# Performance work log

Measured on AMD Instinct MI355X. Metric: run time of the kernel, lower is better.

## Reference

```python
import jax, jax.numpy as jnp
import numpy as np

H_RATIO = 0.33  # matches init_kwargs h_ratio
EPS = 1e-12     # F.normalize default eps


def setup_inputs() -> dict:
    key = jax.random.key(0)
    x = jax.random.normal(key, (64, 2048, 24, 12), dtype=jnp.float32)
    return {"x": x}


def reference(x):
    b, c, h, w = x.shape
    rh = round(H_RATIO * h)  # number of top-energy rows to drop (static)
    # per-sample spatial activation energy, summed over channels: (b, h*w)
    act = jnp.sum(x * x, axis=1).reshape(b, h * w)
    # L2 normalize per sample (faithful to F.normalize; order-preserving anyway)
    norm = jnp.sqrt(jnp.sum(act * act, axis=1, keepdims=True))
    act = act / jnp.maximum(norm, EPS)
    act = act.reshape(b, h, w)
    # per-row max over width -> (b, h); take indices of the rh largest rows
    max_act = jnp.max(act, axis=2)
    ind = jnp.argsort(max_act, axis=1)[:, -rh:]  # (b, rh)
    # row mask: ones everywhere, zero at the top-rh rows per sample
    mask = jnp.ones((b, h), dtype=x.dtype)
    mask = mask.at[jnp.arange(b)[:, None], ind].set(0.0)  # (b, h)
    # broadcast over channels and width (equiv. to the repeat_interleave chain)
    return x * mask[:, None, :, None]
```

## Files before the change

kernel.cpp:

```cpp
#include <hip/hip_runtime.h>

#define B   64
#define C   2048
#define H   24
#define W   12
#define S   (H * W)
#define S4  (S / 4)
#define NCH 32
#define CCH (C / NCH)
#define RH  8

__global__ __launch_bounds__(288) void k_energy_copy(const float* __restrict__ x,
                                                     float* __restrict__ out,
                                                     float* __restrict__ part) {
    const int chunk = blockIdx.x;
    const int b     = blockIdx.y;
    const int t     = threadIdx.x;
    const int f     = t % S4;
    const int g     = t / S4;

    const size_t base4 = (size_t)b * C * S4 + (size_t)chunk * CCH * S4;
    const float4* __restrict__ x4 = (const float4*)x + base4;
    float4* __restrict__       o4 = (float4*)out + base4;

    float4 acc = {0.f, 0.f, 0.f, 0.f};
    #pragma unroll 4
    for (int c = g; c < CCH; c += 4) {
        float4 v = x4[c * S4 + f];
        o4[c * S4 + f] = v;
        acc.x += v.x * v.x;
        acc.y += v.y * v.y;
        acc.z += v.z * v.z;
        acc.w += v.w * v.w;
    }

    __shared__ float4 sm4[4][S4];
    sm4[g][f] = acc;
    __syncthreads();

    const float* sm = (const float*)sm4;
    float sum = sm[0 * S + t] + sm[1 * S + t] + sm[2 * S + t] + sm[3 * S + t];
    part[((size_t)b * NCH + chunk) * S + t] = sum;
}

__global__ __launch_bounds__(288) void k_select(const float* __restrict__ part,
                                                int* __restrict__ drop) {
    const int b = blockIdx.x;
    const int t = threadIdx.x;

    __shared__ float act[S];
    __shared__ float rm[H];

    const float* p = part + (size_t)b * NCH * S + t;
    float sum = 0.f;
    #pragma unroll
    for (int ch = 0; ch < NCH; ch++) sum += p[(size_t)ch * S];
    act[t] = sum;
    __syncthreads();

    if (t < H) {
        float m = act[t * W];
        #pragma unroll
        for (int w = 1; w < W; w++) m = fmaxf(m, act[t * W + w]);
        rm[t] = m;
    }
    __syncthreads();

    if (t < H) {
        const float mt = rm[t];
        int cnt = 0;
        #pragma unroll
        for (int j = 0; j < H; j++) {
            float mj = rm[j];
            if (mj > mt || (mj == mt && j > t)) cnt++;
        }
        drop[b * H + t] = (cnt < RH) ? 1 : 0;
    }
}

__global__ __launch_bounds__(256) void k_zero(float* __restrict__ out,
                                              const int* __restrict__ drop) {
    const int h = blockIdx.x;
    const int b = blockIdx.y;
    if (!drop[b * H + h]) return;

    float4* __restrict__ o4 = (float4*)out + (size_t)b * C * S4 + h * (W / 4);
    const float4 z = {0.f, 0.f, 0.f, 0.f};
    for (int i = threadIdx.x; i < C * (W / 4); i += 256) {
        int c = i / 3;
        int q = i - c * 3;
        o4[(size_t)c * S4 + q] = z;
    }
}

extern "C" void kernel_launch(void* const* d_in, const int* in_sizes, int n_in,
                              void* d_out, int out_size, void* d_ws, size_t ws_size,
                              hipStream_t stream) {
    const float* x   = (const float*)d_in[0];
    float*       out = (float*)d_out;

    float* part = (float*)d_ws;
    int*   drop = (int*)((char*)d_ws + (size_t)B * NCH * S * sizeof(float));

    k_energy_copy<<<dim3(NCH, B), 288, 0, stream>>>(x, out, part);
    k_select<<<B, 288, 0, stream>>>(part, drop);
    k_zero<<<dim3(H, B), 256, 0, stream>>>(out, drop);
}
```

Baseline: 309.1 us.

## Split energy pass from copy and fuse row masking into a second streaming copy

Result: faster. 278.3 us (-10.0%).

```diff
diff --git a/kernel.cpp b/kernel.cpp
--- a/kernel.cpp
+++ b/kernel.cpp
@@ -6,41 +6,38 @@
 #define W   12
 #define S   (H * W)
 #define S4  (S / 4)
+#define W4  (W / 4)
 #define NCH 32
 #define CCH (C / NCH)
 #define RH  8
 
-__global__ __launch_bounds__(288) void k_energy_copy(const float* __restrict__ x,
-                                                     float* __restrict__ out,
-                                                     float* __restrict__ part) {
+typedef float f4 __attribute__((ext_vector_type(4)));
+
+__global__ __launch_bounds__(288) void k_energy(const float* __restrict__ x,
+                                                float* __restrict__ part) {
     const int chunk = blockIdx.x;
     const int b     = blockIdx.y;
     const int t     = threadIdx.x;
     const int f     = t % S4;
     const int g     = t / S4;
 
-    const size_t base4 = (size_t)b * C * S4 + (size_t)chunk * CCH * S4;
-    const float4* __restrict__ x4 = (const float4*)x + base4;
-    float4* __restrict__       o4 = (float4*)out + base4;
+    const f4* __restrict__ x4 =
+        (const f4*)x + (size_t)(b * C + chunk * CCH) * S4;
 
-    float4 acc = {0.f, 0.f, 0.f, 0.f};
-    #pragma unroll 4
-    for (int c = g; c < CCH; c += 4) {
-        float4 v = x4[c * S4 + f];
-        o4[c * S4 + f] = v;
-        acc.x += v.x * v.x;
-        acc.y += v.y * v.y;
-        acc.z += v.z * v.z;
-        acc.w += v.w * v.w;
+    f4 acc = {0.f, 0.f, 0.f, 0.f};
+    #pragma unroll
+    for (int k = 0; k < CCH / 4; ++k) {
+        f4 v = x4[t + S * k];
+        acc += v * v;
     }
 
-    __shared__ float4 sm4[4][S4];
+    __shared__ f4 sm4[4][S4];
     sm4[g][f] = acc;
     __syncthreads();
 
     const float* sm = (const float*)sm4;
-    float sum = sm[0 * S + t] + sm[1 * S + t] + sm[2 * S + t] + sm[3 * S + t];
-    part[((size_t)b * NCH + chunk) * S + t] = sum;
+    part[((size_t)b * NCH + chunk) * S + t] =
+        sm[0 * S + t] + sm[1 * S + t] + sm[2 * S + t] + sm[3 * S + t];
 }
 
 __global__ __launch_bounds__(288) void k_select(const float* __restrict__ part,
@@ -78,18 +75,24 @@
     }
 }
 
-__global__ __launch_bounds__(256) void k_zero(float* __restrict__ out,
-                                              const int* __restrict__ drop) {
-    const int h = blockIdx.x;
-    const int b = blockIdx.y;
-    if (!drop[b * H + h]) return;
+__global__ __launch_bounds__(288) void k_mask_copy(const float* __restrict__ x,
+                                                   float* __restrict__ out,
+                                                   const int* __restrict__ drop) {
+    const int chunk = blockIdx.x;
+    const int b     = blockIdx.y;
+    const int t     = threadIdx.x;
+    const int h     = (t % S4) / W4;
+    const float keep = (drop[b * H + h] == 0) ? 1.0f : 0.0f;
 
-    float4* __restrict__ o4 = (float4*)out + (size_t)b * C * S4 + h * (W / 4);
-    const float4 z = {0.f, 0.f, 0.f, 0.f};
-    for (int i = threadIdx.x; i < C * (W / 4); i += 256) {
-        int c = i / 3;
-        int q = i - c * 3;
-        o4[(size_t)c * S4 + q] = z;
+    const size_t base4 = (size_t)(b * C + chunk * CCH) * S4;
+    const f4* __restrict__ x4 = (const f4*)x + base4;
+    f4* __restrict__       o4 = (f4*)out + base4;
+
+    #pragma unroll
+    for (int k = 0; k < CCH / 4; ++k) {
+        f4 v = x4[t + S * k];
+        f4 r = v * keep;
+        __builtin_nontemporal_store(r, &o4[t + S * k]);
     }
 }
 
@@ -102,7 +105,7 @@
     float* part = (float*)d_ws;
     int*   drop = (int*)((char*)d_ws + (size_t)B * NCH * S * sizeof(float));
 
-    k_energy_copy<<<dim3(NCH, B), 288, 0, stream>>>(x, out, part);
+    k_energy<<<dim3(NCH, B), 288, 0, stream>>>(x, part);
     k_select<<<B, 288, 0, stream>>>(part, drop);
-    k_zero<<<dim3(H, B), 256, 0, stream>>>(out, drop);
+    k_mask_copy<<<dim3(NCH, B), 288, 0, stream>>>(x, out, drop);
 }
```
